# Optimization experiments

Hardware: AMD Instinct MI355X
Metric: run time of the kernel (lower is better)

Reference implementation:

```python
import jax, jax.numpy as jnp
import numpy as np

BN_EPS = 1e-5


def _gru(x, Wih, Whh, bih, bhh):
    # x: [B,S,D]; Wih: [3H,D]; Whh: [3H,H]; PyTorch gate order (r, z, n)
    B, S, D = x.shape
    H = Whh.shape[1]
    xg = jnp.einsum('bsd,gd->bsg', x, Wih) + bih  # [B,S,3H] precomputed input gates

    def step(h, xg_t):
        hg = h @ Whh.T + bhh
        xr, xz, xn = jnp.split(xg_t, 3, axis=-1)
        hr, hz, hn = jnp.split(hg, 3, axis=-1)
        r = jax.nn.sigmoid(xr + hr)
        z = jax.nn.sigmoid(xz + hz)
        n = jnp.tanh(xn + r * hn)
        h_new = (1.0 - z) * n + z * h
        return h_new, h_new

    h0 = jnp.zeros((B, H), x.dtype)
    _, hs = jax.lax.scan(step, h0, jnp.swapaxes(xg, 0, 1))  # [S,B,H]
    return jnp.swapaxes(hs, 0, 1)


def _lstm(x, Wih, Whh, bih, bhh):
    # x: [B,S,D]; PyTorch gate order (i, f, g, o)
    B, S, D = x.shape
    H = Whh.shape[1]
    xg = jnp.einsum('bsd,gd->bsg', x, Wih) + bih  # [B,S,4H]

    def step(carry, xg_t):
        h, c = carry
        g = xg_t + h @ Whh.T + bhh
        i, f, gg, o = jnp.split(g, 4, axis=-1)
        i = jax.nn.sigmoid(i)
        f = jax.nn.sigmoid(f)
        gg = jnp.tanh(gg)
        o = jax.nn.sigmoid(o)
        c_new = f * c + i * gg
        h_new = o * jnp.tanh(c_new)
        return (h_new, c_new), h_new

    h0 = jnp.zeros((B, H), x.dtype)
    c0 = jnp.zeros((B, H), x.dtype)
    _, hs = jax.lax.scan(step, (h0, c0), jnp.swapaxes(xg, 0, 1))
    return jnp.swapaxes(hs, 0, 1)


def setup_inputs() -> dict:
    key = jax.random.key(0)
    B, S, D, H = 64, 512, 40, 512
    ks = jax.random.split(key, 16)
    s_in = 1.0 / np.sqrt(H)

    def u(k, shape):
        return jax.random.uniform(k, shape, jnp.float32, -s_in, s_in)

    inp = {
        'x': jax.random.normal(ks[0], (B, S, D), jnp.float32),
        # rec1: GRU
        'gru_Wih': u(ks[1], (3 * H, D)),
        'gru_Whh': u(ks[2], (3 * H, H)),
        'gru_bih': u(ks[3], (3 * H,)),
        'gru_bhh': u(ks[4], (3 * H,)),
        # rec2: LSTM over [x, ssr] -> input D+1
        'lstm_Wih': u(ks[5], (4 * H, D + 1)),
        'lstm_Whh': u(ks[6], (4 * H, H)),
        'lstm_bih': u(ks[7], (4 * H,)),
        'lstm_bhh': u(ks[8], (4 * H,)),
        # fc1/fc2/fc3: hidden -> 1
        'fc1_w': u(ks[9], (1, H)), 'fc1_b': u(ks[10], (1,)),
        'fc2_w': u(ks[11], (1, H)), 'fc2_b': u(ks[12], (1,)),
        'fc3_w': u(ks[13], (1, H)), 'fc3_b': u(ks[14], (1,)),
        # BatchNorm1d affine params
        'bn_gamma': jnp.ones((H,), jnp.float32),
        'bn_beta': jnp.zeros((H,), jnp.float32),
    }
    return inp


def reference(x, gru_Wih, gru_Whh, gru_bih, gru_bhh,
              lstm_Wih, lstm_Whh, lstm_bih, lstm_bhh,
              fc1_w, fc1_b, fc2_w, fc2_b, fc3_w, fc3_b,
              bn_gamma, bn_beta):
    B, S, D = x.shape
    o1 = _gru(x, gru_Wih, gru_Whh, gru_bih, gru_bhh)  # [B,S,H]
    # BatchNorm1d (training mode): per-channel stats over (batch, time)
    mean = jnp.mean(o1, axis=(0, 1))
    var = jnp.mean((o1 - mean) ** 2, axis=(0, 1))
    o1 = (o1 - mean) * jax.lax.rsqrt(var + BN_EPS) * bn_gamma + bn_beta
    # gated scalar channel (dropout p=0 is identity)
    sr = jax.nn.relu(o1 @ fc1_w.T + fc1_b)            # [B,S,1]
    w = jnp.abs(jax.nn.sigmoid(o1 @ fc2_w.T + fc2_b))  # [B,S,1]
    ssr = sr * (w + 1.0)                              # [B,S,1]
    x2 = jnp.concatenate([x, ssr], axis=2)            # [B,S,D+1]
    o2 = _lstm(x2, lstm_Wih, lstm_Whh, lstm_bih, lstm_bhh)
    out = jax.nn.relu(o2 @ fc3_w.T + fc3_b)           # [B,S,1]
    return out, ssr
```

## Files before the change

kernel.cpp:

```cpp
#include <hip/hip_runtime.h>
#include <stdint.h>

#define MB 16
#define GW 16
#define NU 32
#define HD 512
#define SEQ 512
#define DX 40

using short8 = __attribute__((ext_vector_type(8))) short;
using f32x4  = __attribute__((ext_vector_type(4))) float;

__device__ __forceinline__ unsigned short f2bf(float f) {
  uint32_t u = __builtin_bit_cast(uint32_t, f);
  u += 0x7fffu + ((u >> 16) & 1u);
  return (unsigned short)(u >> 16);
}
__device__ __forceinline__ float bf2f(unsigned short s) {
  uint32_t u = ((uint32_t)s) << 16;
  return __builtin_bit_cast(float, u);
}
__device__ __forceinline__ float sigm(float x) { return 1.0f / (1.0f + __expf(-x)); }


__global__ __launch_bounds__(512, 2) void gru_kernel(
    const float* __restrict__ x, const float* __restrict__ Wih,
    const float* __restrict__ Whh, const float* __restrict__ bih,
    const float* __restrict__ bhh, unsigned* __restrict__ flags,
    unsigned short* __restrict__ hbuf, float* __restrict__ o1,
    float* __restrict__ stats)
{
  const int wg = blockIdx.x & (GW - 1);
  const int g  = blockIdx.x >> 4;
  const int tid = threadIdx.x;
  const int wave = tid >> 6;
  const int lane = tid & 63;
  const int u0 = wg * NU;
  const int bg = g * MB;

  __shared__ unsigned short h_s[MB][520];
  __shared__ unsigned short x_s[MB][72];
  __shared__ float gate_s[3][MB][NU];
  __shared__ float xn_s[MB][NU];
  __shared__ float wn_s[DX][NU];

  for (int i = tid; i < MB * 32; i += 512) x_s[i >> 5][40 + (i & 31)] = 0;
  for (int i = tid; i < DX * NU; i += 512) {
    int c = i >> 5, u = i & 31;
    wn_s[c][u] = Wih[(size_t)(2 * HD + u0 + u) * DX + c];
  }

  short8 bfrag[18];
  const int myGate = wave >> 1;
  const int ut = wave & 1;
  if (wave < 6) {
    const int row = myGate * HD + u0 + ut * 16 + (lane & 15);
    const int kq = (lane >> 4) * 8;
    for (int kt = 0; kt < 16; ++kt) {
      const float* p = Whh + (size_t)row * HD + kt * 32 + kq;
      short8 f;
#pragma unroll
      for (int j = 0; j < 8; ++j) f[j] = (short)f2bf(p[j]);
      bfrag[kt] = f;
    }
    for (int kt = 16; kt < 18; ++kt) {
      short8 f;
#pragma unroll
      for (int j = 0; j < 8; ++j) {
        int c = kt * 32 + kq + j - HD;
        float v = (myGate < 2 && c < DX) ? Wih[(size_t)row * DX + c] : 0.0f;
        f[j] = (short)f2bf(v);
      }
      bfrag[kt] = f;
    }
  }

  const int sb = tid >> 5;
  const int su = tid & 31;
  float hprev = 0.0f, ssum = 0.0f, ssq = 0.0f;
  const float b_r  = bih[u0 + su] + bhh[u0 + su];
  const float b_z  = bih[HD + u0 + su] + bhh[HD + u0 + su];
  const float b_in = bih[2 * HD + u0 + su];
  const float b_hn = bhh[2 * HD + u0 + su];

  unsigned* gf = flags + g * GW * 16;

  for (int t = 0; t < SEQ; ++t) {
    const unsigned long long* hin64 =
        (const unsigned long long*)(hbuf + ((size_t)g * 2 + (t & 1)) * MB * HD);
    uint32_t* hout32 =
        (uint32_t*)(hbuf + ((size_t)g * 2 + ((t + 1) & 1)) * MB * HD);

    {
      int b = tid >> 5, c = tid & 31;
      const float* xr = x + ((size_t)(bg + b) * SEQ + t) * DX;
      x_s[b][c] = f2bf(xr[c]);
      if (c < 8) x_s[b][32 + c] = f2bf(xr[32 + c]);
    }
    if (wave == 0 && lane < GW && lane != wg) {
      const unsigned* f = gf + lane * 16;
      while (__hip_atomic_load(f, __ATOMIC_RELAXED, __HIP_MEMORY_SCOPE_AGENT) <
             (unsigned)t)
        __builtin_amdgcn_s_sleep(1);
    }
    __syncthreads();

    {
#pragma unroll
      for (int it = 0; it < 4; ++it) {
        int q = it * 512 + tid;
        unsigned long long v = __hip_atomic_load(hin64 + q, __ATOMIC_RELAXED,
                                                 __HIP_MEMORY_SCOPE_AGENT);
        int b = q >> 7, c = (q & 127) * 4;
        *(unsigned long long*)(&h_s[b][c]) = v;
      }
    }
    __syncthreads();

    if (wave < 6) {
      const int m = lane & 15;
      const int kq = (lane >> 4) * 8;
      f32x4 acc = {0.f, 0.f, 0.f, 0.f};
#pragma unroll
      for (int kt = 0; kt < 16; ++kt) {
        short8 a = *(const short8*)(&h_s[m][kt * 32 + kq]);
        acc = __builtin_amdgcn_mfma_f32_16x16x32_bf16(a, bfrag[kt], acc, 0, 0, 0);
      }
      short8 ax0 = *(const short8*)(&x_s[m][kq]);
      short8 ax1 = *(const short8*)(&x_s[m][32 + kq]);
      acc = __builtin_amdgcn_mfma_f32_16x16x32_bf16(ax0, bfrag[16], acc, 0, 0, 0);
      acc = __builtin_amdgcn_mfma_f32_16x16x32_bf16(ax1, bfrag[17], acc, 0, 0, 0);
#pragma unroll
      for (int r = 0; r < 4; ++r)
        gate_s[myGate][(lane >> 4) * 4 + r][ut * 16 + (lane & 15)] = acc[r];
    } else {
      int base = (tid - 384) * 4;
#pragma unroll
      for (int i = 0; i < 4; ++i) {
        int idx = base + i, b = idx >> 5, u = idx & 31;
        float s = 0.0f;
        for (int c = 0; c < DX; ++c) s += bf2f(x_s[b][c]) * wn_s[c][u];
        xn_s[b][u] = s;
      }
    }
    __syncthreads();

    float r_ = sigm(gate_s[0][sb][su] + b_r);
    float z_ = sigm(gate_s[1][sb][su] + b_z);
    float n_ = tanhf(xn_s[sb][su] + b_in + r_ * (gate_s[2][sb][su] + b_hn));
    float h = (1.0f - z_) * n_ + z_ * hprev;
    hprev = h;
    ssum += h; ssq += h * h;
    {
      float hp = __shfl_xor(h, 1);
      if ((tid & 1) == 0) {
        uint32_t packed = (uint32_t)f2bf(h) | ((uint32_t)f2bf(hp) << 16);
        __hip_atomic_store(hout32 + ((sb * HD + u0 + su) >> 1), packed,
                           __ATOMIC_RELAXED, __HIP_MEMORY_SCOPE_AGENT);
      }
    }
    __syncthreads();

    if (tid == 0)
      __hip_atomic_store(gf + wg * 16, (unsigned)(t + 1), __ATOMIC_RELAXED,
                         __HIP_MEMORY_SCOPE_AGENT);
    o1[((size_t)(bg + sb) * SEQ + t) * HD + u0 + su] = h;
  }

  atomicAdd(&stats[u0 + su], ssum);
  atomicAdd(&stats[HD + u0 + su], ssq);
}

__global__ __launch_bounds__(512, 2) void lstm_kernel(
    const float* __restrict__ x, const float* __restrict__ Wih,
    const float* __restrict__ Whh, const float* __restrict__ bih,
    const float* __restrict__ bhh, const float* __restrict__ ssr,
    unsigned* __restrict__ flags, unsigned short* __restrict__ hbuf,
    float* __restrict__ o2)
{
  const int wg = blockIdx.x & (GW - 1);
  const int g  = blockIdx.x >> 4;
  const int tid = threadIdx.x;
  const int wave = tid >> 6;
  const int lane = tid & 63;
  const int u0 = wg * NU;
  const int bg = g * MB;

  __shared__ unsigned short h_s[MB][520];
  __shared__ unsigned short x_s[MB][72];
  __shared__ float gate_s[4][MB][NU];

  for (int i = tid; i < MB * 32; i += 512) x_s[i >> 5][40 + (i & 31)] = 0;

  short8 bfrag[18];
  const int myGate = wave >> 1;
  const int ut = wave & 1;
  {
    const int row = myGate * HD + u0 + ut * 16 + (lane & 15);
    const int kq = (lane >> 4) * 8;
    for (int kt = 0; kt < 16; ++kt) {
      const float* p = Whh + (size_t)row * HD + kt * 32 + kq;
      short8 f;
#pragma unroll
      for (int j = 0; j < 8; ++j) f[j] = (short)f2bf(p[j]);
      bfrag[kt] = f;
    }
    for (int kt = 16; kt < 18; ++kt) {
      short8 f;
#pragma unroll
      for (int j = 0; j < 8; ++j) {
        int c = kt * 32 + kq + j - HD;
        float v = (c < 41) ? Wih[(size_t)row * 41 + c] : 0.0f;
        f[j] = (short)f2bf(v);
      }
      bfrag[kt] = f;
    }
  }

  const int sb = tid >> 5;
  const int su = tid & 31;
  float creg = 0.0f;
  const float b_i = bih[u0 + su] + bhh[u0 + su];
  const float b_f = bih[HD + u0 + su] + bhh[HD + u0 + su];
  const float b_g = bih[2 * HD + u0 + su] + bhh[2 * HD + u0 + su];
  const float b_o = bih[3 * HD + u0 + su] + bhh[3 * HD + u0 + su];

  unsigned* gf = flags + g * GW * 16;

  for (int t = 0; t < SEQ; ++t) {
    const unsigned long long* hin64 =
        (const unsigned long long*)(hbuf + ((size_t)g * 2 + (t & 1)) * MB * HD);
    uint32_t* hout32 =
        (uint32_t*)(hbuf + ((size_t)g * 2 + ((t + 1) & 1)) * MB * HD);

    {
      int b = tid >> 5, c = tid & 31;
      const float* xr = x + ((size_t)(bg + b) * SEQ + t) * DX;
      x_s[b][c] = f2bf(xr[c]);
      if (c < 8) x_s[b][32 + c] = f2bf(xr[32 + c]);
      if (c == 8) x_s[b][40] = f2bf(ssr[(size_t)(bg + b) * SEQ + t]);
    }
    if (wave == 0 && lane < GW && lane != wg) {
      const unsigned* f = gf + lane * 16;
      while (__hip_atomic_load(f, __ATOMIC_RELAXED, __HIP_MEMORY_SCOPE_AGENT) <
             (unsigned)t)
        __builtin_amdgcn_s_sleep(1);
    }
    __syncthreads();

    {
#pragma unroll
      for (int it = 0; it < 4; ++it) {
        int q = it * 512 + tid;
        unsigned long long v = __hip_atomic_load(hin64 + q, __ATOMIC_RELAXED,
                                                 __HIP_MEMORY_SCOPE_AGENT);
        int b = q >> 7, c = (q & 127) * 4;
        *(unsigned long long*)(&h_s[b][c]) = v;
      }
    }
    __syncthreads();

    {
      const int m = lane & 15;
      const int kq = (lane >> 4) * 8;
      f32x4 acc = {0.f, 0.f, 0.f, 0.f};
#pragma unroll
      for (int kt = 0; kt < 16; ++kt) {
        short8 a = *(const short8*)(&h_s[m][kt * 32 + kq]);
        acc = __builtin_amdgcn_mfma_f32_16x16x32_bf16(a, bfrag[kt], acc, 0, 0, 0);
      }
      short8 ax0 = *(const short8*)(&x_s[m][kq]);
      short8 ax1 = *(const short8*)(&x_s[m][32 + kq]);
      acc = __builtin_amdgcn_mfma_f32_16x16x32_bf16(ax0, bfrag[16], acc, 0, 0, 0);
      acc = __builtin_amdgcn_mfma_f32_16x16x32_bf16(ax1, bfrag[17], acc, 0, 0, 0);
#pragma unroll
      for (int r = 0; r < 4; ++r)
        gate_s[myGate][(lane >> 4) * 4 + r][ut * 16 + (lane & 15)] = acc[r];
    }
    __syncthreads();

    float gi = sigm(gate_s[0][sb][su] + b_i);
    float gf_ = sigm(gate_s[1][sb][su] + b_f);
    float gg = tanhf(gate_s[2][sb][su] + b_g);
    float go = sigm(gate_s[3][sb][su] + b_o);
    creg = gf_ * creg + gi * gg;
    float h = go * tanhf(creg);
    {
      float hp = __shfl_xor(h, 1);
      if ((tid & 1) == 0) {
        uint32_t packed = (uint32_t)f2bf(h) | ((uint32_t)f2bf(hp) << 16);
        __hip_atomic_store(hout32 + ((sb * HD + u0 + su) >> 1), packed,
                           __ATOMIC_RELAXED, __HIP_MEMORY_SCOPE_AGENT);
      }
    }
    __syncthreads();

    if (tid == 0)
      __hip_atomic_store(gf + wg * 16, (unsigned)(t + 1), __ATOMIC_RELAXED,
                         __HIP_MEMORY_SCOPE_AGENT);
    o2[((size_t)(bg + sb) * SEQ + t) * HD + u0 + su] = h;
  }
}

__global__ __launch_bounds__(512) void coef_kernel(
    const float* __restrict__ stats, const float* __restrict__ fc1_w,
    const float* __restrict__ fc1_b, const float* __restrict__ fc2_w,
    const float* __restrict__ fc2_b, const float* __restrict__ gamma,
    const float* __restrict__ beta, float* __restrict__ coef)
{
  __shared__ float r1[512], r2[512];
  const int j = threadIdx.x;
  const float inv_n = 1.0f / 32768.0f;
  float mean = stats[j] * inv_n;
  float var = stats[HD + j] * inv_n - mean * mean;
  float scale = gamma[j] * rsqrtf(var + 1e-5f);
  float shift = beta[j] - mean * scale;
  coef[j] = fc1_w[j] * scale;
  coef[HD + j] = fc2_w[j] * scale;
  r1[j] = fc1_w[j] * shift;
  r2[j] = fc2_w[j] * shift;
  __syncthreads();
  for (int s = 256; s > 0; s >>= 1) {
    if (j < s) { r1[j] += r1[j + s]; r2[j] += r2[j + s]; }
    __syncthreads();
  }
  if (j == 0) {
    coef[2 * HD] = r1[0] + fc1_b[0];
    coef[2 * HD + 1] = r2[0] + fc2_b[0];
  }
}

__global__ __launch_bounds__(256) void ssr_kernel(
    const float* __restrict__ o1, const float* __restrict__ coef,
    float* __restrict__ ssr_ws, float* __restrict__ dssr)
{
  const int row = blockIdx.x * 4 + (threadIdx.x >> 6);
  const int lane = threadIdx.x & 63;
  const float* p = o1 + (size_t)row * HD + lane * 8;
  float s1 = 0.f, s2 = 0.f;
#pragma unroll
  for (int j = 0; j < 8; ++j) {
    float v = p[j];
    s1 += v * coef[lane * 8 + j];
    s2 += v * coef[HD + lane * 8 + j];
  }
#pragma unroll
  for (int off = 32; off > 0; off >>= 1) {
    s1 += __shfl_down(s1, off);
    s2 += __shfl_down(s2, off);
  }
  if (lane == 0) {
    float sr = fmaxf(s1 + coef[2 * HD], 0.0f);
    float w = fabsf(sigm(s2 + coef[2 * HD + 1]));
    float v = sr * (1.0f + w);
    ssr_ws[row] = v;
    dssr[row] = v;
  }
}

__global__ __launch_bounds__(256) void out_kernel(
    const float* __restrict__ o2, const float* __restrict__ fc3_w,
    const float* __restrict__ fc3_b, float* __restrict__ dout)
{
  const int row = blockIdx.x * 4 + (threadIdx.x >> 6);
  const int lane = threadIdx.x & 63;
  const float* p = o2 + (size_t)row * HD + lane * 8;
  float s = 0.f;
#pragma unroll
  for (int j = 0; j < 8; ++j) s += p[j] * fc3_w[lane * 8 + j];
#pragma unroll
  for (int off = 32; off > 0; off >>= 1) s += __shfl_down(s, off);
  if (lane == 0) dout[row] = fmaxf(s + fc3_b[0], 0.0f);
}

extern "C" void kernel_launch(void* const* d_in, const int* in_sizes, int n_in,
                              void* d_out, int out_size, void* d_ws, size_t ws_size,
                              hipStream_t stream) {
  (void)in_sizes; (void)n_in; (void)out_size; (void)ws_size;
  const float* x    = (const float*)d_in[0];
  const float* gWih = (const float*)d_in[1];
  const float* gWhh = (const float*)d_in[2];
  const float* gbih = (const float*)d_in[3];
  const float* gbhh = (const float*)d_in[4];
  const float* lWih = (const float*)d_in[5];
  const float* lWhh = (const float*)d_in[6];
  const float* lbih = (const float*)d_in[7];
  const float* lbhh = (const float*)d_in[8];
  const float* fc1w = (const float*)d_in[9];
  const float* fc1b = (const float*)d_in[10];
  const float* fc2w = (const float*)d_in[11];
  const float* fc2b = (const float*)d_in[12];
  const float* fc3w = (const float*)d_in[13];
  const float* fc3b = (const float*)d_in[14];
  const float* gam  = (const float*)d_in[15];
  const float* bet  = (const float*)d_in[16];
  float* out = (float*)d_out;

  char* ws = (char*)d_ws;
  unsigned* flags_g = (unsigned*)(ws + 0);
  unsigned* flags_l = (unsigned*)(ws + 4096);
  float* stats      = (float*)(ws + 8192);
  float* coef       = (float*)(ws + 16384);
  float* ssr_ws     = (float*)(ws + 32768);
  unsigned short* hbuf_g = (unsigned short*)(ws + 65536);
  unsigned short* hbuf_l = (unsigned short*)(ws + 196608);
  float* o1 = (float*)(ws + 327680);
  float* o2 = o1 + (size_t)64 * SEQ * HD;

  hipMemsetAsync(ws, 0, 12288, stream);
  hipMemsetAsync(ws + 65536, 0, 262144, stream);

  gru_kernel<<<dim3(64), dim3(512), 0, stream>>>(x, gWih, gWhh, gbih, gbhh,
                                                 flags_g, hbuf_g, o1, stats);
  coef_kernel<<<dim3(1), dim3(512), 0, stream>>>(stats, fc1w, fc1b, fc2w, fc2b,
                                                 gam, bet, coef);
  ssr_kernel<<<dim3(8192), dim3(256), 0, stream>>>(o1, coef, ssr_ws, out + 32768);
  lstm_kernel<<<dim3(64), dim3(512), 0, stream>>>(x, lWih, lWhh, lbih, lbhh, ssr_ws,
                                                  flags_l, hbuf_l, o2);
  out_kernel<<<dim3(8192), dim3(256), 0, stream>>>(o2, fc3w, fc3b, out);
}
```

Before: 3.505 ms.

## Replace per-block flag barrier with timestep-tagged hidden-state words; MFMA for xn

The separate per-workgroup progress flags and extra block barriers are removed. Each hidden-state pair is now written as a 64-bit word carrying its timestep tag, and readers spin on each word until the tag matches, so the data and its readiness arrive together and one __syncthreads per step is dropped. The GRU n-gate input projection moves from a scalar LDS dot-product loop on the spare waves to two bf16 MFMAs. The cost is that the exchange buffer doubles in size and every lane polls individually.

```diff
diff --git a/kernel.cpp b/kernel.cpp
--- a/kernel.cpp
+++ b/kernel.cpp
@@ -7,6 +7,7 @@
 #define HD 512
 #define SEQ 512
 #define DX 40
+#define WPS 4096
 
 using short8 = __attribute__((ext_vector_type(8))) short;
 using f32x4  = __attribute__((ext_vector_type(4))) float;
@@ -16,19 +17,14 @@
   u += 0x7fffu + ((u >> 16) & 1u);
   return (unsigned short)(u >> 16);
 }
-__device__ __forceinline__ float bf2f(unsigned short s) {
-  uint32_t u = ((uint32_t)s) << 16;
-  return __builtin_bit_cast(float, u);
-}
 __device__ __forceinline__ float sigm(float x) { return 1.0f / (1.0f + __expf(-x)); }
 
 
 __global__ __launch_bounds__(512, 2) void gru_kernel(
     const float* __restrict__ x, const float* __restrict__ Wih,
     const float* __restrict__ Whh, const float* __restrict__ bih,
-    const float* __restrict__ bhh, unsigned* __restrict__ flags,
-    unsigned short* __restrict__ hbuf, float* __restrict__ o1,
-    float* __restrict__ stats)
+    const float* __restrict__ bhh, unsigned long long* __restrict__ hbuf,
+    float* __restrict__ o1, float* __restrict__ stats)
 {
   const int wg = blockIdx.x & (GW - 1);
   const int g  = blockIdx.x >> 4;
@@ -42,20 +38,15 @@
   __shared__ unsigned short x_s[MB][72];
   __shared__ float gate_s[3][MB][NU];
   __shared__ float xn_s[MB][NU];
-  __shared__ float wn_s[DX][NU];
 
   for (int i = tid; i < MB * 32; i += 512) x_s[i >> 5][40 + (i & 31)] = 0;
-  for (int i = tid; i < DX * NU; i += 512) {
-    int c = i >> 5, u = i & 31;
-    wn_s[c][u] = Wih[(size_t)(2 * HD + u0 + u) * DX + c];
-  }
 
   short8 bfrag[18];
   const int myGate = wave >> 1;
   const int ut = wave & 1;
+  const int kq = (lane >> 4) * 8;
   if (wave < 6) {
     const int row = myGate * HD + u0 + ut * 16 + (lane & 15);
-    const int kq = (lane >> 4) * 8;
     for (int kt = 0; kt < 16; ++kt) {
       const float* p = Whh + (size_t)row * HD + kt * 32 + kq;
       short8 f;
@@ -70,6 +61,17 @@
         int c = kt * 32 + kq + j - HD;
         float v = (myGate < 2 && c < DX) ? Wih[(size_t)row * DX + c] : 0.0f;
         f[j] = (short)f2bf(v);
+      }
+      bfrag[kt] = f;
+    }
+  } else {
+    const int row = 2 * HD + u0 + (wave - 6) * 16 + (lane & 15);
+    for (int kt = 0; kt < 2; ++kt) {
+      short8 f;
+#pragma unroll
+      for (int j = 0; j < 8; ++j) {
+        int c = kt * 32 + kq + j;
+        f[j] = (short)((c < DX) ? f2bf(Wih[(size_t)row * DX + c]) : 0);
       }
       bfrag[kt] = f;
     }
@@ -83,43 +85,37 @@
   const float b_in = bih[2 * HD + u0 + su];
   const float b_hn = bhh[2 * HD + u0 + su];
 
-  unsigned* gf = flags + g * GW * 16;
-
   for (int t = 0; t < SEQ; ++t) {
-    const unsigned long long* hin64 =
-        (const unsigned long long*)(hbuf + ((size_t)g * 2 + (t & 1)) * MB * HD);
-    uint32_t* hout32 =
-        (uint32_t*)(hbuf + ((size_t)g * 2 + ((t + 1) & 1)) * MB * HD);
-
+    const unsigned long long* slot = hbuf + ((size_t)g * 2 + (t & 1)) * WPS;
+    unsigned long long* oslot      = hbuf + ((size_t)g * 2 + ((t + 1) & 1)) * WPS;
+
+    {
+      unsigned long long w[8];
+#pragma unroll
+      for (int it = 0; it < 8; ++it)
+        w[it] = __hip_atomic_load(slot + it * 512 + tid, __ATOMIC_RELAXED,
+                                  __HIP_MEMORY_SCOPE_AGENT);
+#pragma unroll
+      for (int it = 0; it < 8; ++it) {
+        while ((unsigned)(w[it] >> 32) < (unsigned)t) {
+          __builtin_amdgcn_s_sleep(1);
+          w[it] = __hip_atomic_load(slot + it * 512 + tid, __ATOMIC_RELAXED,
+                                    __HIP_MEMORY_SCOPE_AGENT);
+        }
+        int q = it * 512 + tid;
+        *(uint32_t*)(&h_s[q >> 8][(q & 255) * 2]) = (uint32_t)w[it];
+      }
+    }
     {
       int b = tid >> 5, c = tid & 31;
       const float* xr = x + ((size_t)(bg + b) * SEQ + t) * DX;
       x_s[b][c] = f2bf(xr[c]);
       if (c < 8) x_s[b][32 + c] = f2bf(xr[32 + c]);
     }
-    if (wave == 0 && lane < GW && lane != wg) {
-      const unsigned* f = gf + lane * 16;
-      while (__hip_atomic_load(f, __ATOMIC_RELAXED, __HIP_MEMORY_SCOPE_AGENT) <
-             (unsigned)t)
-        __builtin_amdgcn_s_sleep(1);
-    }
-    __syncthreads();
-
-    {
-#pragma unroll
-      for (int it = 0; it < 4; ++it) {
-        int q = it * 512 + tid;
-        unsigned long long v = __hip_atomic_load(hin64 + q, __ATOMIC_RELAXED,
-                                                 __HIP_MEMORY_SCOPE_AGENT);
-        int b = q >> 7, c = (q & 127) * 4;
-        *(unsigned long long*)(&h_s[b][c]) = v;
-      }
-    }
     __syncthreads();
 
     if (wave < 6) {
       const int m = lane & 15;
-      const int kq = (lane >> 4) * 8;
       f32x4 acc = {0.f, 0.f, 0.f, 0.f};
 #pragma unroll
       for (int kt = 0; kt < 16; ++kt) {
@@ -134,14 +130,15 @@
       for (int r = 0; r < 4; ++r)
         gate_s[myGate][(lane >> 4) * 4 + r][ut * 16 + (lane & 15)] = acc[r];
     } else {
-      int base = (tid - 384) * 4;
-#pragma unroll
-      for (int i = 0; i < 4; ++i) {
-        int idx = base + i, b = idx >> 5, u = idx & 31;
-        float s = 0.0f;
-        for (int c = 0; c < DX; ++c) s += bf2f(x_s[b][c]) * wn_s[c][u];
-        xn_s[b][u] = s;
-      }
+      const int m = lane & 15;
+      f32x4 acc = {0.f, 0.f, 0.f, 0.f};
+      short8 ax0 = *(const short8*)(&x_s[m][kq]);
+      short8 ax1 = *(const short8*)(&x_s[m][32 + kq]);
+      acc = __builtin_amdgcn_mfma_f32_16x16x32_bf16(ax0, bfrag[0], acc, 0, 0, 0);
+      acc = __builtin_amdgcn_mfma_f32_16x16x32_bf16(ax1, bfrag[1], acc, 0, 0, 0);
+#pragma unroll
+      for (int r = 0; r < 4; ++r)
+        xn_s[(lane >> 4) * 4 + r][(wave - 6) * 16 + (lane & 15)] = acc[r];
     }
     __syncthreads();
 
@@ -154,16 +151,13 @@
     {
       float hp = __shfl_xor(h, 1);
       if ((tid & 1) == 0) {
-        uint32_t packed = (uint32_t)f2bf(h) | ((uint32_t)f2bf(hp) << 16);
-        __hip_atomic_store(hout32 + ((sb * HD + u0 + su) >> 1), packed,
+        uint32_t pair = (uint32_t)f2bf(h) | ((uint32_t)f2bf(hp) << 16);
+        unsigned long long w =
+            (unsigned long long)pair | ((unsigned long long)(t + 1) << 32);
+        __hip_atomic_store(oslot + ((sb * HD + u0 + su) >> 1), w,
                            __ATOMIC_RELAXED, __HIP_MEMORY_SCOPE_AGENT);
       }
     }
-    __syncthreads();
-
-    if (tid == 0)
-      __hip_atomic_store(gf + wg * 16, (unsigned)(t + 1), __ATOMIC_RELAXED,
-                         __HIP_MEMORY_SCOPE_AGENT);
     o1[((size_t)(bg + sb) * SEQ + t) * HD + u0 + su] = h;
   }
 
@@ -175,8 +169,7 @@
     const float* __restrict__ x, const float* __restrict__ Wih,
     const float* __restrict__ Whh, const float* __restrict__ bih,
     const float* __restrict__ bhh, const float* __restrict__ ssr,
-    unsigned* __restrict__ flags, unsigned short* __restrict__ hbuf,
-    float* __restrict__ o2)
+    unsigned long long* __restrict__ hbuf, float* __restrict__ o2)
 {
   const int wg = blockIdx.x & (GW - 1);
   const int g  = blockIdx.x >> 4;
@@ -195,9 +188,9 @@
   short8 bfrag[18];
   const int myGate = wave >> 1;
   const int ut = wave & 1;
+  const int kq = (lane >> 4) * 8;
   {
     const int row = myGate * HD + u0 + ut * 16 + (lane & 15);
-    const int kq = (lane >> 4) * 8;
     for (int kt = 0; kt < 16; ++kt) {
       const float* p = Whh + (size_t)row * HD + kt * 32 + kq;
       short8 f;
@@ -225,14 +218,27 @@
   const float b_g = bih[2 * HD + u0 + su] + bhh[2 * HD + u0 + su];
   const float b_o = bih[3 * HD + u0 + su] + bhh[3 * HD + u0 + su];
 
-  unsigned* gf = flags + g * GW * 16;
-
   for (int t = 0; t < SEQ; ++t) {
-    const unsigned long long* hin64 =
-        (const unsigned long long*)(hbuf + ((size_t)g * 2 + (t & 1)) * MB * HD);
-    uint32_t* hout32 =
-        (uint32_t*)(hbuf + ((size_t)g * 2 + ((t + 1) & 1)) * MB * HD);
-
+    const unsigned long long* slot = hbuf + ((size_t)g * 2 + (t & 1)) * WPS;
+    unsigned long long* oslot      = hbuf + ((size_t)g * 2 + ((t + 1) & 1)) * WPS;
+
+    {
+      unsigned long long w[8];
+#pragma unroll
+      for (int it = 0; it < 8; ++it)
+        w[it] = __hip_atomic_load(slot + it * 512 + tid, __ATOMIC_RELAXED,
+                                  __HIP_MEMORY_SCOPE_AGENT);
+#pragma unroll
+      for (int it = 0; it < 8; ++it) {
+        while ((unsigned)(w[it] >> 32) < (unsigned)t) {
+          __builtin_amdgcn_s_sleep(1);
+          w[it] = __hip_atomic_load(slot + it * 512 + tid, __ATOMIC_RELAXED,
+                                    __HIP_MEMORY_SCOPE_AGENT);
+        }
+        int q = it * 512 + tid;
+        *(uint32_t*)(&h_s[q >> 8][(q & 255) * 2]) = (uint32_t)w[it];
+      }
+    }
     {
       int b = tid >> 5, c = tid & 31;
       const float* xr = x + ((size_t)(bg + b) * SEQ + t) * DX;
@@ -240,29 +246,10 @@
       if (c < 8) x_s[b][32 + c] = f2bf(xr[32 + c]);
       if (c == 8) x_s[b][40] = f2bf(ssr[(size_t)(bg + b) * SEQ + t]);
     }
-    if (wave == 0 && lane < GW && lane != wg) {
-      const unsigned* f = gf + lane * 16;
-      while (__hip_atomic_load(f, __ATOMIC_RELAXED, __HIP_MEMORY_SCOPE_AGENT) <
-             (unsigned)t)
-        __builtin_amdgcn_s_sleep(1);
-    }
     __syncthreads();
 
     {
-#pragma unroll
-      for (int it = 0; it < 4; ++it) {
-        int q = it * 512 + tid;
-        unsigned long long v = __hip_atomic_load(hin64 + q, __ATOMIC_RELAXED,
-                                                 __HIP_MEMORY_SCOPE_AGENT);
-        int b = q >> 7, c = (q & 127) * 4;
-        *(unsigned long long*)(&h_s[b][c]) = v;
-      }
-    }
-    __syncthreads();
-
-    {
       const int m = lane & 15;
-      const int kq = (lane >> 4) * 8;
       f32x4 acc = {0.f, 0.f, 0.f, 0.f};
 #pragma unroll
       for (int kt = 0; kt < 16; ++kt) {
@@ -288,16 +275,13 @@
     {
       float hp = __shfl_xor(h, 1);
       if ((tid & 1) == 0) {
-        uint32_t packed = (uint32_t)f2bf(h) | ((uint32_t)f2bf(hp) << 16);
-        __hip_atomic_store(hout32 + ((sb * HD + u0 + su) >> 1), packed,
+        uint32_t pair = (uint32_t)f2bf(h) | ((uint32_t)f2bf(hp) << 16);
+        unsigned long long w =
+            (unsigned long long)pair | ((unsigned long long)(t + 1) << 32);
+        __hip_atomic_store(oslot + ((sb * HD + u0 + su) >> 1), w,
                            __ATOMIC_RELAXED, __HIP_MEMORY_SCOPE_AGENT);
       }
     }
-    __syncthreads();
-
-    if (tid == 0)
-      __hip_atomic_store(gf + wg * 16, (unsigned)(t + 1), __ATOMIC_RELAXED,
-                         __HIP_MEMORY_SCOPE_AGENT);
     o2[((size_t)(bg + sb) * SEQ + t) * HD + u0 + su] = h;
   }
 }
@@ -397,25 +381,23 @@
   float* out = (float*)d_out;
 
   char* ws = (char*)d_ws;
-  unsigned* flags_g = (unsigned*)(ws + 0);
-  unsigned* flags_l = (unsigned*)(ws + 4096);
-  float* stats      = (float*)(ws + 8192);
-  float* coef       = (float*)(ws + 16384);
-  float* ssr_ws     = (float*)(ws + 32768);
-  unsigned short* hbuf_g = (unsigned short*)(ws + 65536);
-  unsigned short* hbuf_l = (unsigned short*)(ws + 196608);
-  float* o1 = (float*)(ws + 327680);
+  float* stats = (float*)(ws + 8192);
+  float* coef  = (float*)(ws + 16384);
+  float* ssr_ws = (float*)(ws + 32768);
+  unsigned long long* hbuf_g = (unsigned long long*)(ws + 262144);
+  unsigned long long* hbuf_l = (unsigned long long*)(ws + 524288);
+  float* o1 = (float*)(ws + 1048576);
   float* o2 = o1 + (size_t)64 * SEQ * HD;
 
-  hipMemsetAsync(ws, 0, 12288, stream);
-  hipMemsetAsync(ws + 65536, 0, 262144, stream);
+  hipMemsetAsync(ws + 8192, 0, 4096, stream);
+  hipMemsetAsync(ws + 262144, 0, 524288, stream);
 
   gru_kernel<<<dim3(64), dim3(512), 0, stream>>>(x, gWih, gWhh, gbih, gbhh,
-                                                 flags_g, hbuf_g, o1, stats);
+                                                 hbuf_g, o1, stats);
   coef_kernel<<<dim3(1), dim3(512), 0, stream>>>(stats, fc1w, fc1b, fc2w, fc2b,
                                                  gam, bet, coef);
   ssr_kernel<<<dim3(8192), dim3(256), 0, stream>>>(o1, coef, ssr_ws, out + 32768);
   lstm_kernel<<<dim3(64), dim3(512), 0, stream>>>(x, lWih, lWhh, lbih, lbhh, ssr_ws,
-                                                  flags_l, hbuf_l, o2);
+                                                  hbuf_l, o2);
   out_kernel<<<dim3(8192), dim3(256), 0, stream>>>(o2, fc3w, fc3b, out);
 }
```

Result: slower. 4.374 ms (+24.8%).

## Per-thread producer flag waits and MFMA for GRU input n-gate

Applied to the files above, without the earlier changes.

Every thread now spins only on the flag of the workgroup that produced the slice of h it loads, then loads that slice right away. This removes the wave-0 wait on all flags and one block barrier per timestep. The GRU's scalar 40-wide input projection for the n gate is replaced by two bf16 MFMAs in the spare waves, with weights held in registers instead of LDS. Workspace offsets are also moved, likely to keep buffers apart. The trade-off is more threads polling global flags and bf16 rounding of the xn weights.

```diff
diff --git a/kernel.cpp b/kernel.cpp
--- a/kernel.cpp
+++ b/kernel.cpp
@@ -15,10 +15,6 @@
   uint32_t u = __builtin_bit_cast(uint32_t, f);
   u += 0x7fffu + ((u >> 16) & 1u);
   return (unsigned short)(u >> 16);
-}
-__device__ __forceinline__ float bf2f(unsigned short s) {
-  uint32_t u = ((uint32_t)s) << 16;
-  return __builtin_bit_cast(float, u);
 }
 __device__ __forceinline__ float sigm(float x) { return 1.0f / (1.0f + __expf(-x)); }
 
@@ -42,20 +38,15 @@
   __shared__ unsigned short x_s[MB][72];
   __shared__ float gate_s[3][MB][NU];
   __shared__ float xn_s[MB][NU];
-  __shared__ float wn_s[DX][NU];
 
   for (int i = tid; i < MB * 32; i += 512) x_s[i >> 5][40 + (i & 31)] = 0;
-  for (int i = tid; i < DX * NU; i += 512) {
-    int c = i >> 5, u = i & 31;
-    wn_s[c][u] = Wih[(size_t)(2 * HD + u0 + u) * DX + c];
-  }
 
   short8 bfrag[18];
   const int myGate = wave >> 1;
   const int ut = wave & 1;
+  const int kq = (lane >> 4) * 8;
   if (wave < 6) {
     const int row = myGate * HD + u0 + ut * 16 + (lane & 15);
-    const int kq = (lane >> 4) * 8;
     for (int kt = 0; kt < 16; ++kt) {
       const float* p = Whh + (size_t)row * HD + kt * 32 + kq;
       short8 f;
@@ -70,6 +61,17 @@
         int c = kt * 32 + kq + j - HD;
         float v = (myGate < 2 && c < DX) ? Wih[(size_t)row * DX + c] : 0.0f;
         f[j] = (short)f2bf(v);
+      }
+      bfrag[kt] = f;
+    }
+  } else {
+    const int row = 2 * HD + u0 + (wave - 6) * 16 + (lane & 15);
+    for (int kt = 0; kt < 2; ++kt) {
+      short8 f;
+#pragma unroll
+      for (int j = 0; j < 8; ++j) {
+        int c = kt * 32 + kq + j;
+        f[j] = (short)((c < DX) ? f2bf(Wih[(size_t)row * DX + c]) : 0);
       }
       bfrag[kt] = f;
     }
@@ -84,6 +86,7 @@
   const float b_hn = bhh[2 * HD + u0 + su];
 
   unsigned* gf = flags + g * GW * 16;
+  unsigned* myProdFlag = gf + ((tid & 127) >> 3) * 16;
 
   for (int t = 0; t < SEQ; ++t) {
     const unsigned long long* hin64 =
@@ -92,34 +95,27 @@
         (uint32_t*)(hbuf + ((size_t)g * 2 + ((t + 1) & 1)) * MB * HD);
 
     {
+      while (__hip_atomic_load(myProdFlag, __ATOMIC_RELAXED,
+                               __HIP_MEMORY_SCOPE_AGENT) < (unsigned)t)
+        __builtin_amdgcn_s_sleep(1);
+#pragma unroll
+      for (int it = 0; it < 4; ++it) {
+        int q = it * 512 + tid;
+        unsigned long long v = __hip_atomic_load(hin64 + q, __ATOMIC_RELAXED,
+                                                 __HIP_MEMORY_SCOPE_AGENT);
+        *(unsigned long long*)(&h_s[q >> 7][(q & 127) * 4]) = v;
+      }
+    }
+    {
       int b = tid >> 5, c = tid & 31;
       const float* xr = x + ((size_t)(bg + b) * SEQ + t) * DX;
       x_s[b][c] = f2bf(xr[c]);
       if (c < 8) x_s[b][32 + c] = f2bf(xr[32 + c]);
     }
-    if (wave == 0 && lane < GW && lane != wg) {
-      const unsigned* f = gf + lane * 16;
-      while (__hip_atomic_load(f, __ATOMIC_RELAXED, __HIP_MEMORY_SCOPE_AGENT) <
-             (unsigned)t)
-        __builtin_amdgcn_s_sleep(1);
-    }
-    __syncthreads();
-
-    {
-#pragma unroll
-      for (int it = 0; it < 4; ++it) {
-        int q = it * 512 + tid;
-        unsigned long long v = __hip_atomic_load(hin64 + q, __ATOMIC_RELAXED,
-                                                 __HIP_MEMORY_SCOPE_AGENT);
-        int b = q >> 7, c = (q & 127) * 4;
-        *(unsigned long long*)(&h_s[b][c]) = v;
-      }
-    }
     __syncthreads();
 
     if (wave < 6) {
       const int m = lane & 15;
-      const int kq = (lane >> 4) * 8;
       f32x4 acc = {0.f, 0.f, 0.f, 0.f};
 #pragma unroll
       for (int kt = 0; kt < 16; ++kt) {
@@ -134,14 +130,15 @@
       for (int r = 0; r < 4; ++r)
         gate_s[myGate][(lane >> 4) * 4 + r][ut * 16 + (lane & 15)] = acc[r];
     } else {
-      int base = (tid - 384) * 4;
-#pragma unroll
-      for (int i = 0; i < 4; ++i) {
-        int idx = base + i, b = idx >> 5, u = idx & 31;
-        float s = 0.0f;
-        for (int c = 0; c < DX; ++c) s += bf2f(x_s[b][c]) * wn_s[c][u];
-        xn_s[b][u] = s;
-      }
+      const int m = lane & 15;
+      f32x4 acc = {0.f, 0.f, 0.f, 0.f};
+      short8 ax0 = *(const short8*)(&x_s[m][kq]);
+      short8 ax1 = *(const short8*)(&x_s[m][32 + kq]);
+      acc = __builtin_amdgcn_mfma_f32_16x16x32_bf16(ax0, bfrag[0], acc, 0, 0, 0);
+      acc = __builtin_amdgcn_mfma_f32_16x16x32_bf16(ax1, bfrag[1], acc, 0, 0, 0);
+#pragma unroll
+      for (int r = 0; r < 4; ++r)
+        xn_s[(lane >> 4) * 4 + r][(wave - 6) * 16 + (lane & 15)] = acc[r];
     }
     __syncthreads();
 
@@ -195,9 +192,9 @@
   short8 bfrag[18];
   const int myGate = wave >> 1;
   const int ut = wave & 1;
+  const int kq = (lane >> 4) * 8;
   {
     const int row = myGate * HD + u0 + ut * 16 + (lane & 15);
-    const int kq = (lane >> 4) * 8;
     for (int kt = 0; kt < 16; ++kt) {
       const float* p = Whh + (size_t)row * HD + kt * 32 + kq;
       short8 f;
@@ -226,6 +223,7 @@
   const float b_o = bih[3 * HD + u0 + su] + bhh[3 * HD + u0 + su];
 
   unsigned* gf = flags + g * GW * 16;
+  unsigned* myProdFlag = gf + ((tid & 127) >> 3) * 16;
 
   for (int t = 0; t < SEQ; ++t) {
     const unsigned long long* hin64 =
@@ -234,35 +232,28 @@
         (uint32_t*)(hbuf + ((size_t)g * 2 + ((t + 1) & 1)) * MB * HD);
 
     {
+      while (__hip_atomic_load(myProdFlag, __ATOMIC_RELAXED,
+                               __HIP_MEMORY_SCOPE_AGENT) < (unsigned)t)
+        __builtin_amdgcn_s_sleep(1);
+#pragma unroll
+      for (int it = 0; it < 4; ++it) {
+        int q = it * 512 + tid;
+        unsigned long long v = __hip_atomic_load(hin64 + q, __ATOMIC_RELAXED,
+                                                 __HIP_MEMORY_SCOPE_AGENT);
+        *(unsigned long long*)(&h_s[q >> 7][(q & 127) * 4]) = v;
+      }
+    }
+    {
       int b = tid >> 5, c = tid & 31;
       const float* xr = x + ((size_t)(bg + b) * SEQ + t) * DX;
       x_s[b][c] = f2bf(xr[c]);
       if (c < 8) x_s[b][32 + c] = f2bf(xr[32 + c]);
       if (c == 8) x_s[b][40] = f2bf(ssr[(size_t)(bg + b) * SEQ + t]);
     }
-    if (wave == 0 && lane < GW && lane != wg) {
-      const unsigned* f = gf + lane * 16;
-      while (__hip_atomic_load(f, __ATOMIC_RELAXED, __HIP_MEMORY_SCOPE_AGENT) <
-             (unsigned)t)
-        __builtin_amdgcn_s_sleep(1);
-    }
-    __syncthreads();
-
-    {
-#pragma unroll
-      for (int it = 0; it < 4; ++it) {
-        int q = it * 512 + tid;
-        unsigned long long v = __hip_atomic_load(hin64 + q, __ATOMIC_RELAXED,
-                                                 __HIP_MEMORY_SCOPE_AGENT);
-        int b = q >> 7, c = (q & 127) * 4;
-        *(unsigned long long*)(&h_s[b][c]) = v;
-      }
-    }
     __syncthreads();
 
     {
       const int m = lane & 15;
-      const int kq = (lane >> 4) * 8;
       f32x4 acc = {0.f, 0.f, 0.f, 0.f};
 #pragma unroll
       for (int kt = 0; kt < 16; ++kt) {
@@ -402,13 +393,13 @@
   float* stats      = (float*)(ws + 8192);
   float* coef       = (float*)(ws + 16384);
   float* ssr_ws     = (float*)(ws + 32768);
-  unsigned short* hbuf_g = (unsigned short*)(ws + 65536);
-  unsigned short* hbuf_l = (unsigned short*)(ws + 196608);
-  float* o1 = (float*)(ws + 327680);
+  unsigned short* hbuf_g = (unsigned short*)(ws + 262144);
+  unsigned short* hbuf_l = (unsigned short*)(ws + 393216);
+  float* o1 = (float*)(ws + 1048576);
   float* o2 = o1 + (size_t)64 * SEQ * HD;
 
   hipMemsetAsync(ws, 0, 12288, stream);
-  hipMemsetAsync(ws + 65536, 0, 262144, stream);
+  hipMemsetAsync(ws + 262144, 0, 262144, stream);
 
   gru_kernel<<<dim3(64), dim3(512), 0, stream>>>(x, gWih, gWhh, gbih, gbhh,
                                                  flags_g, hbuf_g, o1, stats);
```

After: 3.304 ms. 1.06x faster.
